# Kernel optimization log

Hardware: AMD Instinct MI355X
Metric: run time of the kernel (lower is better)

Reference implementation:

```python
import jax, jax.numpy as jnp
import numpy as np

C = 256      # in_channels
NH = 4       # n_heads
NG = 32      # GroupNorm num_groups
EPS = 1e-5   # torch GroupNorm default eps


def _conv1x1(x, w, b):
    # 1x1 conv == per-pixel channel matmul. x: (B,C,H,W), w: (O,C), b: (O,)
    return jnp.einsum('oc,bchw->bohw', w, x) + b[None, :, None, None]


def _groupnorm(x, gamma, beta):
    b, c, h, w = x.shape
    xg = x.reshape(b, NG, c // NG, h, w)
    mu = xg.mean(axis=(2, 3, 4), keepdims=True)
    var = xg.var(axis=(2, 3, 4), keepdims=True)
    xn = ((xg - mu) * jax.lax.rsqrt(var + EPS)).reshape(b, c, h, w)
    return xn * gamma[None, :, None, None] + beta[None, :, None, None]


def setup_inputs() -> dict:
    key = jax.random.key(0)
    ks = jax.random.split(key, 5)
    B, H, W = 2, 64, 64
    s = 1.0 / np.sqrt(C).astype(np.float32)
    return {
        'x': jax.random.normal(ks[0], (B, C, H, W), jnp.float32),
        'gamma': jnp.ones((C,), jnp.float32),
        'beta': jnp.zeros((C,), jnp.float32),
        'wq': jax.random.normal(ks[1], (C, C), jnp.float32) * s,
        'bq': jnp.zeros((C,), jnp.float32),
        'wk': jax.random.normal(ks[2], (C, C), jnp.float32) * s,
        'bk': jnp.zeros((C,), jnp.float32),
        'wv': jax.random.normal(ks[3], (C, C), jnp.float32) * s,
        'bv': jnp.zeros((C,), jnp.float32),
        'wp': jax.random.normal(ks[4], (C, C), jnp.float32) * s,
        'bp': jnp.zeros((C,), jnp.float32),
    }


def reference(x, gamma, beta, wq, bq, wk, bk, wv, bv, wp, bp):
    b, c, h, w = x.shape
    c_ = c // NH  # head dim
    hn = _groupnorm(x, gamma, beta)
    # NOTE: original splits channels as (head_dim, n_heads) with head_dim leading
    q = _conv1x1(hn, wq, bq).reshape(b, c_, NH, h * w)
    k = _conv1x1(hn, wk, bk).reshape(b, c_, NH, h * w)
    v = _conv1x1(hn, wv, bv).reshape(b, c_, NH, h * w)
    scores = jnp.einsum('bcnq,bcnk->bqkn', q, k) * (c_ ** -0.5)  # (B,S,S,NH)
    attn = jax.nn.softmax(scores, axis=2)  # softmax over key axis
    out = jnp.einsum('bcnd,bqdn->bcnq', v, attn).reshape(b, c, h, w)
    return x + _conv1x1(out, wp, bp)
```

## Files before the change

kernel.cpp:

```cpp
#include <hip/hip_runtime.h>

#define CH 256
#define NHEAD 4
#define HD 64
#define SP 4096
#define NB 2
#define QSCALE 0.1803368801111204f

typedef __attribute__((ext_vector_type(8))) short bf16x8;
typedef __attribute__((ext_vector_type(4))) float f32x4;
typedef unsigned int u32;
typedef unsigned short u16;

__device__ inline u16 b16(float f) {
    u32 u = __float_as_uint(f);
    return (u16)((u + 0x8000u) >> 16);
}
__device__ inline u32 bpack(float lo, float hi) {
    u32 ul = __float_as_uint(lo), uh = __float_as_uint(hi);
    return ((uh + 0x8000u) & 0xffff0000u) | ((ul + 0x8000u) >> 16);
}
__device__ inline float fexp2(float x) { return __builtin_amdgcn_exp2f(x); }

__global__ __launch_bounds__(256) void prep_kernel(
    const float* __restrict__ x, float2* __restrict__ part,
    const float* __restrict__ wq, const float* __restrict__ wk,
    const float* __restrict__ wv, const float* __restrict__ wp,
    u16* __restrict__ wqb, u16* __restrict__ wkb,
    u16* __restrict__ wvb, u16* __restrict__ wpb)
{
    int tid = threadIdx.x;
    if (blockIdx.x < 256) {
        int bgq = blockIdx.x;
        int bg = bgq >> 2, qtr = bgq & 3;
        const float4* xp = (const float4*)(x + (size_t)bg * 8 * SP) + qtr * 2048;
        float s = 0.f, ss = 0.f;
        for (int i = tid; i < 2048; i += 256) {
            float4 u = xp[i];
            s  += (u.x + u.y) + (u.z + u.w);
            ss += (u.x * u.x + u.y * u.y) + (u.z * u.z + u.w * u.w);
        }
#pragma unroll
        for (int off = 32; off > 0; off >>= 1) {
            s  += __shfl_down(s, off);
            ss += __shfl_down(ss, off);
        }
        __shared__ float ws_s[4], ws_q[4];
        int w = tid >> 6;
        if ((tid & 63) == 0) { ws_s[w] = s; ws_q[w] = ss; }
        __syncthreads();
        if (tid == 0)
            part[bgq] = make_float2(ws_s[0] + ws_s[1] + ws_s[2] + ws_s[3],
                                    ws_q[0] + ws_q[1] + ws_q[2] + ws_q[3]);
    } else {
        int idx = (blockIdx.x - 256) * 256 + tid;
        int m = idx >> 16, i = idx & 65535;
        if (m == 0)      wqb[i] = b16(wq[i] * QSCALE);
        else if (m == 1) wkb[i] = b16(wk[i]);
        else if (m == 2) wvb[i] = b16(wv[i]);
        else {
            int c = i >> 8, col = i & 255;
            int n = col & 3, d = col >> 2;
            wpb[c * 256 + n * 64 + d] = b16(wp[i]);
        }
    }
}

__global__ __launch_bounds__(256) void qkv_gemm_kernel(
    const float* __restrict__ x, const float2* __restrict__ part,
    const float* __restrict__ gamma, const float* __restrict__ beta,
    const u16* __restrict__ wqb, const u16* __restrict__ wkb,
    const u16* __restrict__ wvb,
    const float* __restrict__ bq, const float* __restrict__ bk,
    const float* __restrict__ bv,
    u16* __restrict__ qt, u16* __restrict__ ktp, u16* __restrict__ vtp)
{
    int zz = blockIdx.y;
    int b = zz / 3, p = zz % 3;
    const u16* W = (p == 0) ? wqb : (p == 1) ? wkb : wvb;
    const float* bias = (p == 0) ? bq : (p == 1) ? bk : bv;
    float bs = (p == 0) ? QSCALE : 1.f;
    int s0 = blockIdx.x * 32;
    int tid = threadIdx.x, w = tid >> 6, lane = tid & 63;
    int t = lane >> 4, ln = lane & 15;

    __shared__ u16 SB[10240];
    __shared__ float As[256], Bs[256];

    {
        int c = tid, bg = b * 32 + (c >> 3);
        float s = 0.f, ss = 0.f;
#pragma unroll
        for (int q = 0; q < 4; q++) { float2 pp = part[bg * 4 + q]; s += pp.x; ss += pp.y; }
        float mu = s * (1.f / 32768.f);
        float var = ss * (1.f / 32768.f) - mu * mu;
        float rs = rsqrtf(var + 1e-5f);
        float ga = gamma[c];
        As[c] = rs * ga;
        Bs[c] = beta[c] - mu * rs * ga;
    }
    __syncthreads();

    {
        int c2 = (tid >> 3) * 2;
        int sseg = (tid & 7) * 4;
#pragma unroll
        for (int it = 0; it < 4; it++) {
            int c = it * 64 + c2;
            float4 v0 = *(const float4*)&x[((size_t)b * CH + c) * SP + s0 + sseg];
            float4 v1 = *(const float4*)&x[((size_t)b * CH + c + 1) * SP + s0 + sseg];
            float a0 = As[c], b0 = Bs[c], a1 = As[c + 1], b1 = Bs[c + 1];
            float e0[4] = {fmaf(a0, v0.x, b0), fmaf(a0, v0.y, b0),
                           fmaf(a0, v0.z, b0), fmaf(a0, v0.w, b0)};
            float e1[4] = {fmaf(a1, v1.x, b1), fmaf(a1, v1.y, b1),
                           fmaf(a1, v1.z, b1), fmaf(a1, v1.w, b1)};
#pragma unroll
            for (int j = 0; j < 4; j++)
                *(u32*)&SB[(sseg + j) * 264 + c] = bpack(e0[j], e1[j]);
        }
    }
    __syncthreads();

    f32x4 acc[4][2];
#pragma unroll
    for (int og = 0; og < 4; og++)
#pragma unroll
        for (int sg = 0; sg < 2; sg++)
            acc[og][sg] = (f32x4){0.f, 0.f, 0.f, 0.f};

#pragma unroll
    for (int ks = 0; ks < 8; ks++) {
        bf16x8 af[4], bfv[2];
#pragma unroll
        for (int og = 0; og < 4; og++)
            af[og] = *(const bf16x8*)&W[(size_t)(w * 64 + og * 16 + ln) * CH + ks * 32 + t * 8];
#pragma unroll
        for (int sg = 0; sg < 2; sg++)
            bfv[sg] = *(const bf16x8*)&SB[(sg * 16 + ln) * 264 + ks * 32 + t * 8];
#pragma unroll
        for (int og = 0; og < 4; og++)
#pragma unroll
            for (int sg = 0; sg < 2; sg++)
                acc[og][sg] = __builtin_amdgcn_mfma_f32_16x16x32_bf16(
                    af[og], bfv[sg], acc[og][sg], 0, 0, 0);
    }
    __syncthreads();

    if (p < 2) {
#pragma unroll
        for (int og = 0; og < 4; og++)
#pragma unroll
            for (int sg = 0; sg < 2; sg++)
#pragma unroll
                for (int r = 0; r < 4; r++) {
                    int o = w * 64 + og * 16 + 4 * t + r;
                    SB[(r * 32 + sg * 16 + ln) * 72 + (w * 16 + og * 4 + t)] =
                        b16(acc[og][sg][r] + bias[o] * bs);
                }
        __syncthreads();
        if (p == 0) {
#pragma unroll
            for (int it = 0; it < 4; it++) {
                int f = it * 256 + tid;
                int o8 = f & 7, sl = (f >> 3) & 31, n = f >> 8;
                *(uint4*)&qt[((size_t)(b * 4 + n) * SP + s0 + sl) * HD + o8 * 8] =
                    *(const uint4*)&SB[(n * 32 + sl) * 72 + o8 * 8];
            }
        } else {
#pragma unroll
            for (int it = 0; it < 4; it++) {
                int f = it * 256 + tid;
                int o8 = f & 7, sl = (f >> 3) & 31, n = f >> 8;
                int key = s0 + sl;
                int g = ((key >> 4) & 3) * 2 + (o8 >> 2);
                int lp = (key & 15) + 16 * (o8 & 3);
                *(uint4*)&ktp[(size_t)(b * 4 + n) * SP * HD +
                              (size_t)(key >> 6) * 4096 + g * 512 + lp * 8] =
                    *(const uint4*)&SB[(n * 32 + sl) * 72 + o8 * 8];
            }
        }
    } else {
#pragma unroll
        for (int og = 0; og < 4; og++)
#pragma unroll
            for (int sg = 0; sg < 2; sg++)
#pragma unroll
                for (int r = 0; r < 4; r++) {
                    int o = w * 64 + og * 16 + 4 * t + r;
                    SB[(r * 64 + w * 16 + og * 4 + t) * 40 + sg * 16 + ln] =
                        b16(acc[og][sg][r] + bias[o]);
                }
        __syncthreads();
#pragma unroll
        for (int it = 0; it < 4; it++) {
            int f = it * 256 + tid;
            int so8 = f & 3, d = (f >> 2) & 63, n = f >> 8;
            int key = s0 + so8 * 8;
            int g = ((d >> 4) & 3) * 2 + ((key >> 5) & 1);
            int lp = (d & 15) + 16 * ((key >> 3) & 3);
            *(uint4*)&vtp[(size_t)(b * 4 + n) * SP * HD +
                          (size_t)(key >> 6) * 4096 + g * 512 + lp * 8] =
                *(const uint4*)&SB[(n * 64 + d) * 40 + so8 * 8];
        }
    }
}

template <int NT>
__global__ __launch_bounds__(256, 3) void attn_kernel(
    const u16* __restrict__ qtb, const u16* __restrict__ ktp,
    const u16* __restrict__ vtp, u16* __restrict__ opart,
    float* __restrict__ lpart)
{
    int bx = blockIdx.x;
    int z = bx & 7, qt_i = (bx >> 3) & 31, sp = bx >> 8;
    int sq0 = qt_i * 128;
    int tile0 = sp * NT;
    const u16* qz = qtb + (size_t)z * SP * HD;
    const u16* kz = ktp + (size_t)z * SP * HD;
    const u16* vz = vtp + (size_t)z * SP * HD;

    int tid = threadIdx.x, w = tid >> 6, l = tid & 63;
    int t = l >> 4, ln = l & 15;

    __shared__ __align__(16) u32 Pb[4][2][512];

    bf16x8 qf[2][2];
#pragma unroll
    for (int qg = 0; qg < 2; qg++)
#pragma unroll
        for (int ds = 0; ds < 2; ds++)
            qf[qg][ds] = *(const bf16x8*)&qz[
                (size_t)(sq0 + w * 32 + qg * 16 + ln) * HD + ds * 32 + t * 8];

    bf16x8 kf[8], vf[8];
#pragma unroll
    for (int g = 0; g < 8; g++)
        kf[g] = *(const bf16x8*)&kz[(size_t)tile0 * 4096 + g * 512 + l * 8];

    float lsum[2] = {0.f, 0.f};
    f32x4 oacc[2][4];
#pragma unroll
    for (int qg = 0; qg < 2; qg++)
#pragma unroll
        for (int dg = 0; dg < 4; dg++)
            oacc[qg][dg] = (f32x4){0.f, 0.f, 0.f, 0.f};

    const f32x4 z4 = {0.f, 0.f, 0.f, 0.f};
    f32x4 sa[2][4];

    auto ep = [&](int qg) {
#pragma unroll
        for (int kg = 0; kg < 4; kg++) {
            float e0 = fexp2(sa[qg][kg][0]);
            float e1 = fexp2(sa[qg][kg][1]);
            float e2 = fexp2(sa[qg][kg][2]);
            float e3 = fexp2(sa[qg][kg][3]);
            lsum[qg] += (e0 + e1) + (e2 + e3);
            u32 p0 = __builtin_amdgcn_perm(__float_as_uint(e1), __float_as_uint(e0), 0x07060302u);
            u32 p1 = __builtin_amdgcn_perm(__float_as_uint(e3), __float_as_uint(e2), 0x07060302u);
            int Lt = ln + 16 * (2 * (kg & 1) + (t >> 1));
            int ksg = kg >> 1;
            *(uint2*)&Pb[w][qg][(ksg * 64 + Lt) * 4 + 2 * (t & 1)] =
                make_uint2(p0, p1);
        }
    };

#pragma unroll
    for (int kti = 0; kti < NT; kti++) {
        size_t tb = (size_t)(tile0 + kti) * 4096;

#pragma unroll
        for (int g = 0; g < 8; g++)
            vf[g] = *(const bf16x8*)&vz[tb + g * 512 + l * 8];

#pragma unroll
        for (int kg = 0; kg < 4; kg++)
#pragma unroll
            for (int qg = 0; qg < 2; qg++)
                sa[qg][kg] = __builtin_amdgcn_mfma_f32_16x16x32_bf16(
                    kf[kg * 2 + 0], qf[qg][0], z4, 0, 0, 0);
#pragma unroll
        for (int kg = 0; kg < 4; kg++)
#pragma unroll
            for (int qg = 0; qg < 2; qg++)
                sa[qg][kg] = __builtin_amdgcn_mfma_f32_16x16x32_bf16(
                    kf[kg * 2 + 1], qf[qg][1], sa[qg][kg], 0, 0, 0);

        if (kti < NT - 1) {
            size_t nb = tb + 4096;
#pragma unroll
            for (int g = 0; g < 8; g++)
                kf[g] = *(const bf16x8*)&kz[nb + g * 512 + l * 8];
        }

        ep(0);
#pragma unroll
        for (int qg = 0; qg < 2; qg++) {
            if (qg == 0) ep(1);
            bf16x8 pf[2];
#pragma unroll
            for (int ksg = 0; ksg < 2; ksg++)
                pf[ksg] = *(const bf16x8*)&Pb[w][qg][(ksg * 64 + l) * 4];
#pragma unroll
            for (int ksg = 0; ksg < 2; ksg++)
#pragma unroll
                for (int dg = 0; dg < 4; dg++)
                    oacc[qg][dg] = __builtin_amdgcn_mfma_f32_16x16x32_bf16(
                        pf[ksg], vf[dg * 2 + ksg], oacc[qg][dg], 0, 0, 0);
        }
    }

#pragma unroll
    for (int qg = 0; qg < 2; qg++) {
        lsum[qg] += __shfl_xor(lsum[qg], 16);
        lsum[qg] += __shfl_xor(lsum[qg], 32);
    }

    size_t obase = (size_t)(sp * 8 + z) * SP;
    u16* po = (u16*)&Pb[w][0][0];
#pragma unroll
    for (int qg = 0; qg < 2; qg++)
#pragma unroll
        for (int dg = 0; dg < 4; dg++)
#pragma unroll
            for (int r = 0; r < 4; r++)
                po[(qg * 16 + 4 * t + r) * 64 + dg * 16 + ln] = b16(oacc[qg][dg][r]);
#pragma unroll
    for (int i = 0; i < 4; i++) {
        int f = i * 512 + l * 8;
        int qloc = f >> 6, d0 = f & 63;
        uint4 v = *(const uint4*)&po[f];
        *(uint4*)&opart[(obase + sq0 + w * 32 + qloc) * HD + d0] = v;
    }
    if (t == 0)
#pragma unroll
        for (int qg = 0; qg < 2; qg++)
            lpart[obase + sq0 + w * 32 + qg * 16 + ln] = lsum[qg];
}

template <int NSPLIT>
__global__ __launch_bounds__(256) void proj_gemm_kernel(
    const u16* __restrict__ opart, const float* __restrict__ lpart,
    const u16* __restrict__ wpb, const float* __restrict__ bp,
    const float* __restrict__ x, float* __restrict__ out)
{
    int b = blockIdx.y;
    int s0 = blockIdx.x * 16;
    int tid = threadIdx.x, w = tid >> 6, lane = tid & 63;
    int t = lane >> 4, ln = lane & 15;

    __shared__ u16 BsL[16 * 264];

#pragma unroll
    for (int it = 0; it < 2; it++) {
        int f = it * 256 + tid;
        int oct = f & 31, s = f >> 5;
        int n = oct >> 3, d0 = (oct & 7) * 8;
        float lsumv = 0.f;
        float accv[8] = {0.f,0.f,0.f,0.f,0.f,0.f,0.f,0.f};
#pragma unroll
        for (int sp = 0; sp < NSPLIT; sp++) {
            size_t base = (size_t)(sp * 8 + b * 4 + n) * SP + s0 + s;
            lsumv += lpart[base];
            uint4 o4 = *(const uint4*)&opart[base * HD + d0];
            u32 ov[4] = {o4.x, o4.y, o4.z, o4.w};
#pragma unroll
            for (int i = 0; i < 4; i++) {
                accv[2 * i + 0] += __uint_as_float(ov[i] << 16);
                accv[2 * i + 1] += __uint_as_float(ov[i] & 0xffff0000u);
            }
        }
        float inv = 1.f / lsumv;
        u32 res[4];
#pragma unroll
        for (int i = 0; i < 4; i++)
            res[i] = (bpack(accv[2 * i + 0] * inv, accv[2 * i + 1] * inv));
        *(uint4*)&BsL[s * 264 + oct * 8] = make_uint4(res[0], res[1], res[2], res[3]);
    }
    __syncthreads();

    f32x4 acc[4];
#pragma unroll
    for (int og = 0; og < 4; og++)
        acc[og] = (f32x4){0.f, 0.f, 0.f, 0.f};

#pragma unroll
    for (int ks = 0; ks < 8; ks++) {
        bf16x8 af[4];
#pragma unroll
        for (int og = 0; og < 4; og++)
            af[og] = *(const bf16x8*)&wpb[(size_t)(w * 64 + og * 16 + ln) * CH + ks * 32 + t * 8];
        bf16x8 bfv = *(const bf16x8*)&BsL[ln * 264 + ks * 32 + t * 8];
#pragma unroll
        for (int og = 0; og < 4; og++)
            acc[og] = __builtin_amdgcn_mfma_f32_16x16x32_bf16(
                af[og], bfv, acc[og], 0, 0, 0);
    }

#pragma unroll
    for (int og = 0; og < 4; og++)
#pragma unroll
        for (int r = 0; r < 4; r++) {
            int c = w * 64 + og * 16 + 4 * t + r;
            size_t idx = ((size_t)b * CH + c) * SP + s0 + ln;
            out[idx] = acc[og][r] + bp[c] + x[idx];
        }
}

extern "C" void kernel_launch(void* const* d_in, const int* in_sizes, int n_in,
                              void* d_out, int out_size, void* d_ws, size_t ws_size,
                              hipStream_t stream)
{
    const float* x     = (const float*)d_in[0];
    const float* gamma = (const float*)d_in[1];
    const float* beta  = (const float*)d_in[2];
    const float* wq = (const float*)d_in[3]; const float* bq = (const float*)d_in[4];
    const float* wk = (const float*)d_in[5]; const float* bk = (const float*)d_in[6];
    const float* wv = (const float*)d_in[7]; const float* bv = (const float*)d_in[8];
    const float* wp = (const float*)d_in[9]; const float* bp = (const float*)d_in[10];
    float* out = (float*)d_out;

    const size_t TEN = (size_t)8 * SP * HD;
    const size_t NEED8 = 4096 + 524288 + 3 * TEN * 2 + 8 * TEN * 2 + 8 * 8 * SP * 4;
    int nsplit = (ws_size >= NEED8) ? 8 : 4;

    char* wsb = (char*)d_ws;
    float2* part = (float2*)wsb;
    u16* wqb = (u16*)(wsb + 4096);
    u16* wkb = wqb + 65536;
    u16* wvb = wkb + 65536;
    u16* wpb = wvb + 65536;
    u16* qt  = wpb + 65536;
    u16* ktp = qt + TEN;
    u16* vtp = ktp + TEN;
    u16* opart = vtp + TEN;
    float* lpart = (float*)(opart + (size_t)nsplit * TEN);

    prep_kernel<<<dim3(1280), dim3(256), 0, stream>>>(
        x, part, wq, wk, wv, wp, wqb, wkb, wvb, wpb);
    qkv_gemm_kernel<<<dim3(128, 6), dim3(256), 0, stream>>>(
        x, part, gamma, beta, wqb, wkb, wvb, bq, bk, bv, qt, ktp, vtp);
    if (nsplit == 8) {
        attn_kernel<8><<<dim3(2048), dim3(256), 0, stream>>>(
            qt, ktp, vtp, opart, lpart);
        proj_gemm_kernel<8><<<dim3(256, 2), dim3(256), 0, stream>>>(
            opart, lpart, wpb, bp, x, out);
    } else {
        attn_kernel<16><<<dim3(1024), dim3(256), 0, stream>>>(
            qt, ktp, vtp, opart, lpart);
        proj_gemm_kernel<4><<<dim3(256, 2), dim3(256), 0, stream>>>(
            opart, lpart, wpb, bp, x, out);
    }
}
```

Before: 155.0 us.

## Double per-block query tile in attention and merge prep kernel work

The attention kernel now processes 256 queries per block (64 per wave, four query groups) instead of 128. It splits each 64-key tile into two halves with separate K register sets, which halves the number of blocks and doubles the reuse of each K/V load. Launch bounds drop from 3 to 2 blocks per CU to make room for the larger accumulator state. The prep kernel is folded into 256 blocks that each do the groupnorm partial sums and also a strided share of the weight conversion. The risks are lower occupancy from register pressure and fewer blocks to fill the GPU.

```diff
diff --git a/kernel.cpp b/kernel.cpp
--- a/kernel.cpp
+++ b/kernel.cpp
@@ -4,7 +4,6 @@
 #define NHEAD 4
 #define HD 64
 #define SP 4096
-#define NB 2
 #define QSCALE 0.1803368801111204f
 
 typedef __attribute__((ext_vector_type(8))) short bf16x8;
@@ -30,30 +29,31 @@
     u16* __restrict__ wvb, u16* __restrict__ wpb)
 {
     int tid = threadIdx.x;
-    if (blockIdx.x < 256) {
-        int bgq = blockIdx.x;
-        int bg = bgq >> 2, qtr = bgq & 3;
-        const float4* xp = (const float4*)(x + (size_t)bg * 8 * SP) + qtr * 2048;
-        float s = 0.f, ss = 0.f;
-        for (int i = tid; i < 2048; i += 256) {
-            float4 u = xp[i];
-            s  += (u.x + u.y) + (u.z + u.w);
-            ss += (u.x * u.x + u.y * u.y) + (u.z * u.z + u.w * u.w);
-        }
-#pragma unroll
-        for (int off = 32; off > 0; off >>= 1) {
-            s  += __shfl_down(s, off);
-            ss += __shfl_down(ss, off);
-        }
-        __shared__ float ws_s[4], ws_q[4];
-        int w = tid >> 6;
-        if ((tid & 63) == 0) { ws_s[w] = s; ws_q[w] = ss; }
-        __syncthreads();
-        if (tid == 0)
-            part[bgq] = make_float2(ws_s[0] + ws_s[1] + ws_s[2] + ws_s[3],
-                                    ws_q[0] + ws_q[1] + ws_q[2] + ws_q[3]);
-    } else {
-        int idx = (blockIdx.x - 256) * 256 + tid;
+    int bgq = blockIdx.x;
+    int bg = bgq >> 2, qtr = bgq & 3;
+    const float4* xp = (const float4*)(x + (size_t)bg * 8 * SP) + qtr * 2048;
+    float s = 0.f, ss = 0.f;
+    for (int i = tid; i < 2048; i += 256) {
+        float4 u = xp[i];
+        s  += (u.x + u.y) + (u.z + u.w);
+        ss += (u.x * u.x + u.y * u.y) + (u.z * u.z + u.w * u.w);
+    }
+#pragma unroll
+    for (int off = 32; off > 0; off >>= 1) {
+        s  += __shfl_down(s, off);
+        ss += __shfl_down(ss, off);
+    }
+    __shared__ float ws_s[4], ws_q[4];
+    int w = tid >> 6;
+    if ((tid & 63) == 0) { ws_s[w] = s; ws_q[w] = ss; }
+    __syncthreads();
+    if (tid == 0)
+        part[bgq] = make_float2(ws_s[0] + ws_s[1] + ws_s[2] + ws_s[3],
+                                ws_q[0] + ws_q[1] + ws_q[2] + ws_q[3]);
+
+#pragma unroll
+    for (int j = 0; j < 4; j++) {
+        int idx = blockIdx.x * 1024 + j * 256 + tid;
         int m = idx >> 16, i = idx & 65535;
         if (m == 0)      wqb[i] = b16(wq[i] * QSCALE);
         else if (m == 1) wkb[i] = b16(wk[i]);
@@ -102,8 +102,7 @@
     __syncthreads();
 
     {
-        int c2 = (tid >> 3) * 2;
-        int sseg = (tid & 7) * 4;
+        int c2 = (tid >> 3) * 2, sseg = (tid & 7) * 4;
 #pragma unroll
         for (int it = 0; it < 4; it++) {
             int c = it * 64 + c2;
@@ -206,14 +205,14 @@
 }
 
 template <int NT>
-__global__ __launch_bounds__(256, 3) void attn_kernel(
+__global__ __launch_bounds__(256, 2) void attn_kernel(
     const u16* __restrict__ qtb, const u16* __restrict__ ktp,
     const u16* __restrict__ vtp, u16* __restrict__ opart,
     float* __restrict__ lpart)
 {
     int bx = blockIdx.x;
-    int z = bx & 7, qt_i = (bx >> 3) & 31, sp = bx >> 8;
-    int sq0 = qt_i * 128;
+    int z = bx & 7, qt_i = (bx >> 3) & 15, sp = bx >> 7;
+    int sq0 = qt_i * 256;
     int tile0 = sp * NT;
     const u16* qz = qtb + (size_t)z * SP * HD;
     const u16* kz = ktp + (size_t)z * SP * HD;
@@ -222,35 +221,35 @@
     int tid = threadIdx.x, w = tid >> 6, l = tid & 63;
     int t = l >> 4, ln = l & 15;
 
-    __shared__ __align__(16) u32 Pb[4][2][512];
-
-    bf16x8 qf[2][2];
-#pragma unroll
-    for (int qg = 0; qg < 2; qg++)
+    __shared__ __align__(16) u32 Pb[4][4][256];
+
+    bf16x8 qf[4][2];
+#pragma unroll
+    for (int qg = 0; qg < 4; qg++)
 #pragma unroll
         for (int ds = 0; ds < 2; ds++)
             qf[qg][ds] = *(const bf16x8*)&qz[
-                (size_t)(sq0 + w * 32 + qg * 16 + ln) * HD + ds * 32 + t * 8];
-
-    bf16x8 kf[8], vf[8];
-#pragma unroll
-    for (int g = 0; g < 8; g++)
-        kf[g] = *(const bf16x8*)&kz[(size_t)tile0 * 4096 + g * 512 + l * 8];
-
-    float lsum[2] = {0.f, 0.f};
-    f32x4 oacc[2][4];
-#pragma unroll
-    for (int qg = 0; qg < 2; qg++)
+                (size_t)(sq0 + w * 64 + qg * 16 + ln) * HD + ds * 32 + t * 8];
+
+    bf16x8 kfA[4], kfB[4], vf[4];
+#pragma unroll
+    for (int i = 0; i < 4; i++)
+        kfA[i] = *(const bf16x8*)&kz[(size_t)tile0 * 4096 + i * 512 + l * 8];
+
+    float lsum[4] = {0.f, 0.f, 0.f, 0.f};
+    f32x4 oacc[4][4];
+#pragma unroll
+    for (int qg = 0; qg < 4; qg++)
 #pragma unroll
         for (int dg = 0; dg < 4; dg++)
             oacc[qg][dg] = (f32x4){0.f, 0.f, 0.f, 0.f};
 
     const f32x4 z4 = {0.f, 0.f, 0.f, 0.f};
-    f32x4 sa[2][4];
+    f32x4 sa[4][2];
 
     auto ep = [&](int qg) {
 #pragma unroll
-        for (int kg = 0; kg < 4; kg++) {
+        for (int kg = 0; kg < 2; kg++) {
             float e0 = fexp2(sa[qg][kg][0]);
             float e1 = fexp2(sa[qg][kg][1]);
             float e2 = fexp2(sa[qg][kg][2]);
@@ -258,11 +257,35 @@
             lsum[qg] += (e0 + e1) + (e2 + e3);
             u32 p0 = __builtin_amdgcn_perm(__float_as_uint(e1), __float_as_uint(e0), 0x07060302u);
             u32 p1 = __builtin_amdgcn_perm(__float_as_uint(e3), __float_as_uint(e2), 0x07060302u);
-            int Lt = ln + 16 * (2 * (kg & 1) + (t >> 1));
-            int ksg = kg >> 1;
-            *(uint2*)&Pb[w][qg][(ksg * 64 + Lt) * 4 + 2 * (t & 1)] =
-                make_uint2(p0, p1);
-        }
+            int Lt = ln + 16 * (kg * 2 + (t >> 1));
+            *(uint2*)&Pb[w][qg][Lt * 4 + 2 * (t & 1)] = make_uint2(p0, p1);
+        }
+    };
+
+    auto half = [&](const bf16x8* kf, int h) {
+#pragma unroll
+        for (int kg = 0; kg < 2; kg++)
+#pragma unroll
+            for (int qg = 0; qg < 4; qg++)
+                sa[qg][kg] = __builtin_amdgcn_mfma_f32_16x16x32_bf16(
+                    kf[kg * 2 + 0], qf[qg][0], z4, 0, 0, 0);
+#pragma unroll
+        for (int kg = 0; kg < 2; kg++)
+#pragma unroll
+            for (int qg = 0; qg < 4; qg++)
+                sa[qg][kg] = __builtin_amdgcn_mfma_f32_16x16x32_bf16(
+                    kf[kg * 2 + 1], qf[qg][1], sa[qg][kg], 0, 0, 0);
+        ep(0);
+#pragma unroll
+        for (int qg = 0; qg < 4; qg++) {
+            if (qg < 3) ep(qg + 1);
+            bf16x8 pf = *(const bf16x8*)&Pb[w][qg][l * 4];
+#pragma unroll
+            for (int dg = 0; dg < 4; dg++)
+                oacc[qg][dg] = __builtin_amdgcn_mfma_f32_16x16x32_bf16(
+                    pf, vf[dg], oacc[qg][dg], 0, 0, 0);
+        }
+        (void)h;
     };
 
 #pragma unroll
@@ -270,48 +293,68 @@
         size_t tb = (size_t)(tile0 + kti) * 4096;
 
 #pragma unroll
-        for (int g = 0; g < 8; g++)
-            vf[g] = *(const bf16x8*)&vz[tb + g * 512 + l * 8];
-
-#pragma unroll
-        for (int kg = 0; kg < 4; kg++)
-#pragma unroll
-            for (int qg = 0; qg < 2; qg++)
+        for (int dg = 0; dg < 4; dg++)
+            vf[dg] = *(const bf16x8*)&vz[tb + (dg * 2 + 0) * 512 + l * 8];
+#pragma unroll
+        for (int kg = 0; kg < 2; kg++)
+#pragma unroll
+            for (int qg = 0; qg < 4; qg++)
                 sa[qg][kg] = __builtin_amdgcn_mfma_f32_16x16x32_bf16(
-                    kf[kg * 2 + 0], qf[qg][0], z4, 0, 0, 0);
-#pragma unroll
-        for (int kg = 0; kg < 4; kg++)
-#pragma unroll
-            for (int qg = 0; qg < 2; qg++)
+                    kfA[kg * 2 + 0], qf[qg][0], z4, 0, 0, 0);
+#pragma unroll
+        for (int kg = 0; kg < 2; kg++)
+#pragma unroll
+            for (int qg = 0; qg < 4; qg++)
                 sa[qg][kg] = __builtin_amdgcn_mfma_f32_16x16x32_bf16(
-                    kf[kg * 2 + 1], qf[qg][1], sa[qg][kg], 0, 0, 0);
-
+                    kfA[kg * 2 + 1], qf[qg][1], sa[qg][kg], 0, 0, 0);
+#pragma unroll
+        for (int i = 0; i < 4; i++)
+            kfB[i] = *(const bf16x8*)&kz[tb + (4 + i) * 512 + l * 8];
+        ep(0);
+#pragma unroll
+        for (int qg = 0; qg < 4; qg++) {
+            if (qg < 3) ep(qg + 1);
+            bf16x8 pf = *(const bf16x8*)&Pb[w][qg][l * 4];
+#pragma unroll
+            for (int dg = 0; dg < 4; dg++)
+                oacc[qg][dg] = __builtin_amdgcn_mfma_f32_16x16x32_bf16(
+                    pf, vf[dg], oacc[qg][dg], 0, 0, 0);
+        }
+
+#pragma unroll
+        for (int dg = 0; dg < 4; dg++)
+            vf[dg] = *(const bf16x8*)&vz[tb + (dg * 2 + 1) * 512 + l * 8];
+#pragma unroll
+        for (int kg = 0; kg < 2; kg++)
+#pragma unroll
+            for (int qg = 0; qg < 4; qg++)
+                sa[qg][kg] = __builtin_amdgcn_mfma_f32_16x16x32_bf16(
+                    kfB[kg * 2 + 0], qf[qg][0], z4, 0, 0, 0);
+#pragma unroll
+        for (int kg = 0; kg < 2; kg++)
+#pragma unroll
+            for (int qg = 0; qg < 4; qg++)
+                sa[qg][kg] = __builtin_amdgcn_mfma_f32_16x16x32_bf16(
+                    kfB[kg * 2 + 1], qf[qg][1], sa[qg][kg], 0, 0, 0);
         if (kti < NT - 1) {
-            size_t nb = tb + 4096;
-#pragma unroll
-            for (int g = 0; g < 8; g++)
-                kf[g] = *(const bf16x8*)&kz[nb + g * 512 + l * 8];
-        }
-
+#pragma unroll
+            for (int i = 0; i < 4; i++)
+                kfA[i] = *(const bf16x8*)&kz[tb + 4096 + i * 512 + l * 8];
+        }
         ep(0);
 #pragma unroll
-        for (int qg = 0; qg < 2; qg++) {
-            if (qg == 0) ep(1);
-            bf16x8 pf[2];
-#pragma unroll
-            for (int ksg = 0; ksg < 2; ksg++)
-                pf[ksg] = *(const bf16x8*)&Pb[w][qg][(ksg * 64 + l) * 4];
-#pragma unroll
-            for (int ksg = 0; ksg < 2; ksg++)
-#pragma unroll
-                for (int dg = 0; dg < 4; dg++)
-                    oacc[qg][dg] = __builtin_amdgcn_mfma_f32_16x16x32_bf16(
-                        pf[ksg], vf[dg * 2 + ksg], oacc[qg][dg], 0, 0, 0);
-        }
-    }
-
-#pragma unroll
-    for (int qg = 0; qg < 2; qg++) {
+        for (int qg = 0; qg < 4; qg++) {
+            if (qg < 3) ep(qg + 1);
+            bf16x8 pf = *(const bf16x8*)&Pb[w][qg][l * 4];
+#pragma unroll
+            for (int dg = 0; dg < 4; dg++)
+                oacc[qg][dg] = __builtin_amdgcn_mfma_f32_16x16x32_bf16(
+                    pf, vf[dg], oacc[qg][dg], 0, 0, 0);
+        }
+    }
+
+#pragma unroll
+    for (int qg = 0; qg < 4; qg++) {
         lsum[qg] += __shfl_xor(lsum[qg], 16);
         lsum[qg] += __shfl_xor(lsum[qg], 32);
     }
@@ -319,23 +362,28 @@
     size_t obase = (size_t)(sp * 8 + z) * SP;
     u16* po = (u16*)&Pb[w][0][0];
 #pragma unroll
-    for (int qg = 0; qg < 2; qg++)
-#pragma unroll
-        for (int dg = 0; dg < 4; dg++)
-#pragma unroll
-            for (int r = 0; r < 4; r++)
-                po[(qg * 16 + 4 * t + r) * 64 + dg * 16 + ln] = b16(oacc[qg][dg][r]);
-#pragma unroll
-    for (int i = 0; i < 4; i++) {
-        int f = i * 512 + l * 8;
-        int qloc = f >> 6, d0 = f & 63;
-        uint4 v = *(const uint4*)&po[f];
-        *(uint4*)&opart[(obase + sq0 + w * 32 + qloc) * HD + d0] = v;
+    for (int pass = 0; pass < 2; pass++) {
+#pragma unroll
+        for (int qh = 0; qh < 2; qh++) {
+            int qg = pass * 2 + qh;
+#pragma unroll
+            for (int dg = 0; dg < 4; dg++)
+#pragma unroll
+                for (int r = 0; r < 4; r++)
+                    po[(qh * 16 + 4 * t + r) * 64 + dg * 16 + ln] = b16(oacc[qg][dg][r]);
+        }
+#pragma unroll
+        for (int i = 0; i < 4; i++) {
+            int f = i * 512 + l * 8;
+            int qloc = f >> 6, d0 = f & 63;
+            uint4 v = *(const uint4*)&po[f];
+            *(uint4*)&opart[(obase + sq0 + w * 64 + pass * 32 + qloc) * HD + d0] = v;
+        }
     }
     if (t == 0)
 #pragma unroll
-        for (int qg = 0; qg < 2; qg++)
-            lpart[obase + sq0 + w * 32 + qg * 16 + ln] = lsum[qg];
+        for (int qg = 0; qg < 4; qg++)
+            lpart[obase + sq0 + w * 64 + qg * 16 + ln] = lsum[qg];
 }
 
 template <int NSPLIT>
@@ -374,7 +422,7 @@
         u32 res[4];
 #pragma unroll
         for (int i = 0; i < 4; i++)
-            res[i] = (bpack(accv[2 * i + 0] * inv, accv[2 * i + 1] * inv));
+            res[i] = bpack(accv[2 * i + 0] * inv, accv[2 * i + 1] * inv);
         *(uint4*)&BsL[s * 264 + oct * 8] = make_uint4(res[0], res[1], res[2], res[3]);
     }
     __syncthreads();
@@ -436,17 +484,17 @@
     u16* opart = vtp + TEN;
     float* lpart = (float*)(opart + (size_t)nsplit * TEN);
 
-    prep_kernel<<<dim3(1280), dim3(256), 0, stream>>>(
+    prep_kernel<<<dim3(256), dim3(256), 0, stream>>>(
         x, part, wq, wk, wv, wp, wqb, wkb, wvb, wpb);
     qkv_gemm_kernel<<<dim3(128, 6), dim3(256), 0, stream>>>(
         x, part, gamma, beta, wqb, wkb, wvb, bq, bk, bv, qt, ktp, vtp);
     if (nsplit == 8) {
-        attn_kernel<8><<<dim3(2048), dim3(256), 0, stream>>>(
+        attn_kernel<8><<<dim3(1024), dim3(256), 0, stream>>>(
             qt, ktp, vtp, opart, lpart);
         proj_gemm_kernel<8><<<dim3(256, 2), dim3(256), 0, stream>>>(
             opart, lpart, wpb, bp, x, out);
     } else {
-        attn_kernel<16><<<dim3(1024), dim3(256), 0, stream>>>(
+        attn_kernel<16><<<dim3(512), dim3(256), 0, stream>>>(
             qt, ktp, vtp, opart, lpart);
         proj_gemm_kernel<4><<<dim3(256, 2), dim3(256), 0, stream>>>(
             opart, lpart, wpb, bp, x, out);
```

Measured after the change: 153.3 us. About the same (-1.1%).
